# Kernel optimization log

Hardware: AMD Instinct MI355X
Metric: run time of the kernel (lower is better)

The kernel has to match this reference:

```python
import jax, jax.numpy as jnp
import numpy as np

SCALE_POS = 2.0
SCALE_NEG = 40.0
THRESH_POS = 0.5
THRESH_NEG = 0.5
MARGIN = 0.1
EPS = 1e-5


def setup_inputs() -> dict:
    key = jax.random.key(0)
    kf, kl = jax.random.split(key)
    B, D, NUM_CLASSES = 4096, 1024, 64
    feats = jax.random.normal(kf, (B, D), dtype=jnp.float32)
    feats = feats / jnp.linalg.norm(feats, axis=1, keepdims=True)  # L2-normalized embeddings
    labels = jax.random.randint(kl, (B,), 0, NUM_CLASSES, dtype=jnp.int64)
    return {"feats": feats, "labels": labels}


def reference(feats, labels):
    B = feats.shape[0]
    sim = jnp.matmul(feats, feats.T)  # [B, B]
    same = labels[:, None] == labels[None, :]
    pos_mask = same & (sim < 1.0 - EPS)  # drop self / near-duplicate pairs
    neg_mask = ~same

    # hard mining: keep negatives above min positive - margin, positives below max negative + margin
    min_pos = jnp.min(jnp.where(pos_mask, sim, jnp.inf), axis=1)   # [B]
    max_neg = jnp.max(jnp.where(neg_mask, sim, -jnp.inf), axis=1)  # [B]
    neg_sel = neg_mask & (sim + MARGIN > min_pos[:, None])
    pos_sel = pos_mask & (sim - MARGIN < max_neg[:, None])

    pos_sum = jnp.sum(jnp.where(pos_sel, jnp.exp(-SCALE_POS * (sim - THRESH_POS)), 0.0), axis=1)
    neg_sum = jnp.sum(jnp.where(neg_sel, jnp.exp(SCALE_NEG * (sim - THRESH_NEG)), 0.0), axis=1)
    pos_loss = jnp.log1p(pos_sum) / SCALE_POS
    neg_loss = jnp.log1p(neg_sum) / SCALE_NEG

    valid = jnp.any(pos_sel, axis=1) & jnp.any(neg_sel, axis=1)  # rows skipped by original loop
    return jnp.sum(jnp.where(valid, pos_loss + neg_loss, 0.0)) / B
```

## Files before the change

### kernel.cpp

```cpp
#include <hip/hip_runtime.h>

typedef _Float16 half8 __attribute__((ext_vector_type(8)));
typedef float floatx4 __attribute__((ext_vector_type(4)));
typedef int intx4 __attribute__((ext_vector_type(4)));
typedef int intx8 __attribute__((ext_vector_type(8)));
typedef __attribute__((address_space(1))) const void gvoid;
typedef __attribute__((address_space(3))) void svoid;

#define SCALE_POS 2.0f
#define SCALE_NEG 40.0f
#define THRESH 0.5f
#define MARGIN 0.1f
#define EPSV 1e-5f

__global__ void k_init(const float* __restrict__ feats,
                       unsigned char* __restrict__ f8,
                       float* __restrict__ out,
                       int total4) {
    int i = blockIdx.x * blockDim.x + threadIdx.x;
    if (i < total4) {
        float4 v = ((const float4*)feats)[i];
        int w = 0;
        w = __builtin_amdgcn_cvt_pk_fp8_f32(v.x, v.y, w, false);
        w = __builtin_amdgcn_cvt_pk_fp8_f32(v.z, v.w, w, true);
        ((int*)f8)[i] = w;
    }
    if (i == 0) out[0] = 0.f;
}

__global__ void __launch_bounds__(256, 4)
k_gemm_h(const unsigned char* __restrict__ f8,
         const int* __restrict__ labels,
         float* __restrict__ pmin,
         float* __restrict__ pmax,
         _Float16* __restrict__ simh,
         int D, int nb) {
    __shared__ __align__(16) unsigned char As[128 * 128];
    __shared__ __align__(16) unsigned char Bs[128 * 128];
    __shared__ int labR[128], labC[128];

    const int bid0 = blockIdx.x;
    const int t = (bid0 & 7) * 66 + (bid0 >> 3);
    int rb = 0, rem = t;
    while (rem >= nb - rb) { rem -= nb - rb; ++rb; }
    const int cb = rb + rem;
    const int rowBase = rb * 128;
    const int colBase = cb * 128;

    const int tid = threadIdx.x;
    const int lane = tid & 63;
    const int wave = tid >> 6;
    const int wr = wave >> 1;
    const int wc = wave & 1;
    const int q = lane >> 4;
    const int cIn = lane & 15;

    if (tid < 128) labR[tid] = labels[rowBase + tid];
    else           labC[tid - 128] = labels[colBase + (tid - 128)];

    const int subrow = lane >> 3;
    const int swz = (lane & 7) ^ subrow;
    const unsigned char* gP[8];
    unsigned char* lP[8];
#pragma unroll
    for (int j = 0; j < 8; ++j) {
        const int c = wave * 8 + j;
        const int grow = (c < 16) ? (rowBase + c * 8 + subrow)
                                  : (colBase + (c - 16) * 8 + subrow);
        gP[j] = f8 + (size_t)grow * D + swz * 16;
        lP[j] = ((c < 16) ? (As + c * 1024) : (Bs + (c - 16) * 1024)) + lane * 16;
    }

    int aOff0[4], aOff1[4], bOff0[4], bOff1[4];
#pragma unroll
    for (int i = 0; i < 4; ++i) {
        const int rA = wr * 64 + i * 16 + cIn;
        aOff0[i] = rA * 128 + ((2 * q) ^ (rA & 7)) * 16;
        aOff1[i] = rA * 128 + ((2 * q + 1) ^ (rA & 7)) * 16;
        const int rB = wc * 64 + i * 16 + cIn;
        bOff0[i] = rB * 128 + ((2 * q) ^ (rB & 7)) * 16;
        bOff1[i] = rB * 128 + ((2 * q + 1) ^ (rB & 7)) * 16;
    }

    floatx4 acc[4][4] = {};

    const int KT = D >> 7;
    for (int kt = 0; kt < KT; ++kt) {
        const int kOff = kt * 128;
        __syncthreads();
#pragma unroll
        for (int j = 0; j < 8; ++j)
            __builtin_amdgcn_global_load_lds((gvoid*)(gP[j] + kOff), (svoid*)lP[j], 16, 0, 0);
        __syncthreads();

        intx8 a[4], b[4];
#pragma unroll
        for (int i = 0; i < 4; ++i) {
            intx4 lo = *(const intx4*)(As + aOff0[i]);
            intx4 hi = *(const intx4*)(As + aOff1[i]);
            a[i] = __builtin_shufflevector(lo, hi, 0, 1, 2, 3, 4, 5, 6, 7);
        }
#pragma unroll
        for (int i = 0; i < 4; ++i) {
            intx4 lo = *(const intx4*)(Bs + bOff0[i]);
            intx4 hi = *(const intx4*)(Bs + bOff1[i]);
            b[i] = __builtin_shufflevector(lo, hi, 0, 1, 2, 3, 4, 5, 6, 7);
        }
#pragma unroll
        for (int i = 0; i < 4; ++i)
#pragma unroll
            for (int j2 = 0; j2 < 4; ++j2)
                acc[i][j2] = __builtin_amdgcn_mfma_scale_f32_16x16x128_f8f6f4(
                    a[i], b[j2], acc[i][j2], 0, 0,
                    0, 0x7f7f7f7f,
                    0, 0x7f7f7f7f);
    }

    int rLabv[16];
#pragma unroll
    for (int mi = 0; mi < 4; ++mi)
#pragma unroll
        for (int rr = 0; rr < 4; ++rr)
            rLabv[mi * 4 + rr] = labR[wr * 64 + mi * 16 + q * 4 + rr];
    int cLabv[4];
#pragma unroll
    for (int ni = 0; ni < 4; ++ni)
        cLabv[ni] = labC[wc * 64 + ni * 16 + cIn];

    {
        half8* dst = (half8*)(simh + (size_t)(2 * t + wc) * 8192
                                   + (size_t)(wr * 64 + lane) * 64);
#pragma unroll
        for (int mi = 0; mi < 4; ++mi) {
            half8 h0, h1;
#pragma unroll
            for (int ni = 0; ni < 2; ++ni)
#pragma unroll
                for (int rr = 0; rr < 4; ++rr) {
                    h0[ni * 4 + rr] = (_Float16)acc[mi][ni][rr];
                    h1[ni * 4 + rr] = (_Float16)acc[mi][ni + 2][rr];
                }
            dst[mi * 2] = h0;
            dst[mi * 2 + 1] = h1;
        }
    }

    {
        const int slotR = 2 * cb + wc;
#pragma unroll
        for (int mi = 0; mi < 4; ++mi)
#pragma unroll
            for (int rr = 0; rr < 4; ++rr) {
                const int rLoc = wr * 64 + mi * 16 + q * 4 + rr;
                const int rLab = rLabv[mi * 4 + rr];
                float vmin = 1e30f, vmax = -1e30f;
#pragma unroll
                for (int ni = 0; ni < 4; ++ni) {
                    float s = acc[mi][ni][rr];
                    if (rLab == cLabv[ni]) {
                        if (s < 1.0f - EPSV) vmin = fminf(vmin, s);
                    } else {
                        vmax = fmaxf(vmax, s);
                    }
                }
#pragma unroll
                for (int off = 8; off; off >>= 1) {
                    vmin = fminf(vmin, __shfl_xor(vmin, off, 16));
                    vmax = fmaxf(vmax, __shfl_xor(vmax, off, 16));
                }
                if (cIn == 0) {
                    pmin[(size_t)(rowBase + rLoc) * 64 + slotR] = vmin;
                    pmax[(size_t)(rowBase + rLoc) * 64 + slotR] = vmax;
                }
            }
    }

    if (rb != cb) {
        const int slotC = 2 * rb + wr;
#pragma unroll
        for (int ni = 0; ni < 4; ++ni) {
            const int cLab = cLabv[ni];
            float vmin = 1e30f, vmax = -1e30f;
#pragma unroll
            for (int mi = 0; mi < 4; ++mi)
#pragma unroll
                for (int rr = 0; rr < 4; ++rr) {
                    float s = acc[mi][ni][rr];
                    if (rLabv[mi * 4 + rr] == cLab) {
                        if (s < 1.0f - EPSV) vmin = fminf(vmin, s);
                    } else {
                        vmax = fmaxf(vmax, s);
                    }
                }
            vmin = fminf(vmin, __shfl_xor(vmin, 16, 64));
            vmin = fminf(vmin, __shfl_xor(vmin, 32, 64));
            vmax = fmaxf(vmax, __shfl_xor(vmax, 16, 64));
            vmax = fmaxf(vmax, __shfl_xor(vmax, 32, 64));
            if (q == 0) {
                const int cLoc = wc * 64 + ni * 16 + cIn;
                pmin[(size_t)(colBase + cLoc) * 64 + slotC] = vmin;
                pmax[(size_t)(colBase + cLoc) * 64 + slotC] = vmax;
            }
        }
    }
}

__global__ void __launch_bounds__(256)
k_sum2f(const _Float16* __restrict__ simh,
        const int* __restrict__ labels,
        const float* __restrict__ pmin,
        const float* __restrict__ pmax,
        float* __restrict__ psP, float* __restrict__ psN,
        int nb, int B) {
    __shared__ int labR[128], labC[128];
    __shared__ float gNR[128], gPR[128], gNC[128], gPC[128];

    int t = blockIdx.x;
    int rb = 0, rem = t;
    while (rem >= nb - rb) { rem -= nb - rb; ++rb; }
    const int cb = rb + rem;
    const int rowBase = rb * 128;

    const int tid = threadIdx.x;
    const int sub = tid >> 7;
    const int stid = tid & 127;
    const int wave = stid >> 6;
    const int lane = tid & 63;
    const int q = lane >> 4;
    const int cIn = lane & 15;
    const int colBase = cb * 128 + sub * 64;

    {
        const int j = tid & 127;
        const int base = (tid < 128) ? (rowBase + j) : (cb * 128 + j);
        const floatx4* pm = (const floatx4*)(pmin + (size_t)base * 64);
        const floatx4* px = (const floatx4*)(pmax + (size_t)base * 64);
        float mn = 1e30f, mx = -1e30f;
#pragma unroll
        for (int k = 0; k < 16; ++k) {
            floatx4 a = pm[k];
            floatx4 b = px[k];
            mn = fminf(mn, fminf(fminf(a[0], a[1]), fminf(a[2], a[3])));
            mx = fmaxf(mx, fmaxf(fmaxf(b[0], b[1]), fmaxf(b[2], b[3])));
        }
        if (tid < 128) {
            labR[j] = labels[rowBase + j];
            gNR[j] = mn - MARGIN;
            gPR[j] = mx + MARGIN;
        } else {
            labC[j] = labels[cb * 128 + j];
            gNC[j] = mn - MARGIN;
            gPC[j] = mx + MARGIN;
        }
    }
    __syncthreads();

    int cLabv[4];
    float gNCv[4], gPCv[4];
#pragma unroll
    for (int ni = 0; ni < 4; ++ni) {
        const int j = sub * 64 + ni * 16 + cIn;
        cLabv[ni] = labC[j];
        gNCv[ni] = gNC[j];
        gPCv[ni] = gPC[j];
    }

    const half8* src = (const half8*)(simh + (size_t)(2 * t + sub) * 8192 + (size_t)stid * 64);
    half8 hv[8];
#pragma unroll
    for (int v = 0; v < 8; ++v) hv[v] = src[v];

    float cps[4] = {}, cns[4] = {};
    const bool offd = (rb != cb);

    const int slotR = 2 * cb + sub;

#pragma unroll
    for (int mi = 0; mi < 4; ++mi)
#pragma unroll
        for (int rr = 0; rr < 4; ++rr) {
            const int rLoc = wave * 64 + mi * 16 + q * 4 + rr;
            const int rLab = labR[rLoc];
            const float gn = gNR[rLoc];
            const float gp = gPR[rLoc];
            float rp = 0.f, rn = 0.f;
#pragma unroll
            for (int ni = 0; ni < 4; ++ni) {
                const int idx = mi * 16 + ni * 4 + rr;
                const float s = (float)hv[idx >> 3][idx & 7];
                if (rLab == cLabv[ni]) {
                    if (s < 1.0f - EPSV) {
                        float ev = __expf(-SCALE_POS * (s - THRESH));
                        if (s < gp) rp += ev;
                        if (offd && s < gPCv[ni]) cps[ni] += ev;
                    }
                } else {
                    float ev = __expf(SCALE_NEG * (s - THRESH));
                    if (s > gn) rn += ev;
                    if (offd && s > gNCv[ni]) cns[ni] += ev;
                }
            }
#pragma unroll
            for (int off = 8; off; off >>= 1) {
                rp += __shfl_xor(rp, off, 16);
                rn += __shfl_xor(rn, off, 16);
            }
            if (cIn == 0) {
                psP[(size_t)(rowBase + rLoc) * 64 + slotR] = rp;
                psN[(size_t)(rowBase + rLoc) * 64 + slotR] = rn;
            }
        }
    if (offd) {
        const int slotC = 2 * rb + wave;
#pragma unroll
        for (int ni = 0; ni < 4; ++ni) {
            cps[ni] += __shfl_xor(cps[ni], 16, 64);
            cps[ni] += __shfl_xor(cps[ni], 32, 64);
            cns[ni] += __shfl_xor(cns[ni], 16, 64);
            cns[ni] += __shfl_xor(cns[ni], 32, 64);
            if (q == 0) {
                const int cLoc = ni * 16 + cIn;
                psP[(size_t)(colBase + cLoc) * 64 + slotC] = cps[ni];
                psN[(size_t)(colBase + cLoc) * 64 + slotC] = cns[ni];
            }
        }
    }
}

__global__ void __launch_bounds__(256)
k_final(const float* __restrict__ psP, const float* __restrict__ psN,
        float* __restrict__ out, int B) {
    __shared__ float red[4];
    const int r = blockIdx.x * 256 + threadIdx.x;
    const floatx4* pp = (const floatx4*)(psP + (size_t)r * 64);
    const floatx4* pn = (const floatx4*)(psN + (size_t)r * 64);
    float P = 0.f, N = 0.f;
#pragma unroll
    for (int k = 0; k < 16; ++k) {
        floatx4 a = pp[k];
        P += (a[0] + a[1]) + (a[2] + a[3]);
        floatx4 b = pn[k];
        N += (b[0] + b[1]) + (b[2] + b[3]);
    }
    float a = (P > 0.f && N > 0.f)
                  ? log1pf(P) * (1.0f / SCALE_POS) + log1pf(N) * (1.0f / SCALE_NEG)
                  : 0.f;
#pragma unroll
    for (int off = 32; off; off >>= 1) a += __shfl_down(a, off, 64);
    const int tid = threadIdx.x;
    if ((tid & 63) == 0) red[tid >> 6] = a;
    __syncthreads();
    if (tid == 0)
        atomicAdd(out, (red[0] + red[1] + red[2] + red[3]) / (float)B);
}

extern "C" void kernel_launch(void* const* d_in, const int* in_sizes, int n_in,
                              void* d_out, int out_size, void* d_ws, size_t ws_size,
                              hipStream_t stream) {
    const float* feats = (const float*)d_in[0];
    const int* labels = (const int*)d_in[1];
    const int B = in_sizes[1];
    const int D = in_sizes[0] / B;
    const int nb = B / 128;
    const int NT = nb * (nb + 1) / 2;
    const int total4 = B * D / 4;

    char* ws = (char*)d_ws;
    unsigned char* f8 = (unsigned char*)ws;
    size_t off = (size_t)B * D;
    float* pmin = (float*)(ws + off); off += (size_t)64 * B * 4;
    float* pmax = (float*)(ws + off); off += (size_t)64 * B * 4;
    float* psP  = (float*)(ws + off); off += (size_t)64 * B * 4;
    float* psN  = (float*)(ws + off); off += (size_t)64 * B * 4;
    _Float16* simh = (_Float16*)(ws + ((off + 255) & ~(size_t)255));
    float* outp = (float*)d_out;

    k_init<<<(total4 + 255) / 256, 256, 0, stream>>>(feats, f8, outp, total4);

    k_gemm_h<<<NT, 256, 0, stream>>>(f8, labels, pmin, pmax, simh, D, nb);

    k_sum2f<<<NT, 256, 0, stream>>>(simh, labels, pmin, pmax, psP, psN, nb, B);

    k_final<<<B / 256, 256, 0, stream>>>(psP, psN, outp, B);
}
```

Baseline: 136.3 us.

## Recompute FP8 similarity GEMM in second pass instead of storing fp16 tiles

The first GEMM pass no longer writes the fp16 similarity matrix to global memory. A second kernel recomputes the same FP8 MFMA tile GEMM and applies the exp-sum mining directly on the accumulators. This trades roughly 32MB of fp16 write plus read traffic for a second K-loop of matrix math. The second pass also sums the fp32 accumulators instead of fp16-rounded values, so precision slightly improves.

```diff
diff --git a/kernel.cpp b/kernel.cpp
--- a/kernel.cpp
+++ b/kernel.cpp
@@ -1,6 +1,5 @@
 #include <hip/hip_runtime.h>
 
-typedef _Float16 half8 __attribute__((ext_vector_type(8)));
 typedef float floatx4 __attribute__((ext_vector_type(4)));
 typedef int intx4 __attribute__((ext_vector_type(4)));
 typedef int intx8 __attribute__((ext_vector_type(8)));
@@ -29,12 +28,11 @@
 }
 
 __global__ void __launch_bounds__(256, 4)
-k_gemm_h(const unsigned char* __restrict__ f8,
-         const int* __restrict__ labels,
-         float* __restrict__ pmin,
-         float* __restrict__ pmax,
-         _Float16* __restrict__ simh,
-         int D, int nb) {
+k_gemmA(const unsigned char* __restrict__ f8,
+        const int* __restrict__ labels,
+        float* __restrict__ pmin,
+        float* __restrict__ pmax,
+        int D, int nb) {
     __shared__ __align__(16) unsigned char As[128 * 128];
     __shared__ __align__(16) unsigned char Bs[128 * 128];
     __shared__ int labR[128], labC[128];
@@ -112,8 +110,7 @@
             for (int j2 = 0; j2 < 4; ++j2)
                 acc[i][j2] = __builtin_amdgcn_mfma_scale_f32_16x16x128_f8f6f4(
                     a[i], b[j2], acc[i][j2], 0, 0,
-                    0, 0x7f7f7f7f,
-                    0, 0x7f7f7f7f);
+                    0, 0x7f7f7f7f, 0, 0x7f7f7f7f);
     }
 
     int rLabv[16];
@@ -126,24 +123,6 @@
 #pragma unroll
     for (int ni = 0; ni < 4; ++ni)
         cLabv[ni] = labC[wc * 64 + ni * 16 + cIn];
-
-    {
-        half8* dst = (half8*)(simh + (size_t)(2 * t + wc) * 8192
-                                   + (size_t)(wr * 64 + lane) * 64);
-#pragma unroll
-        for (int mi = 0; mi < 4; ++mi) {
-            half8 h0, h1;
-#pragma unroll
-            for (int ni = 0; ni < 2; ++ni)
-#pragma unroll
-                for (int rr = 0; rr < 4; ++rr) {
-                    h0[ni * 4 + rr] = (_Float16)acc[mi][ni][rr];
-                    h1[ni * 4 + rr] = (_Float16)acc[mi][ni + 2][rr];
-                }
-            dst[mi * 2] = h0;
-            dst[mi * 2 + 1] = h1;
-        }
-    }
 
     {
         const int slotR = 2 * cb + wc;
@@ -205,34 +184,38 @@
     }
 }
 
-__global__ void __launch_bounds__(256)
-k_sum2f(const _Float16* __restrict__ simh,
+__global__ void __launch_bounds__(256, 4)
+k_gemmB(const unsigned char* __restrict__ f8,
         const int* __restrict__ labels,
         const float* __restrict__ pmin,
         const float* __restrict__ pmax,
-        float* __restrict__ psP, float* __restrict__ psN,
-        int nb, int B) {
+        float* __restrict__ psP,
+        float* __restrict__ psN,
+        int D, int nb) {
+    __shared__ __align__(16) unsigned char As[128 * 128];
+    __shared__ __align__(16) unsigned char Bs[128 * 128];
     __shared__ int labR[128], labC[128];
     __shared__ float gNR[128], gPR[128], gNC[128], gPC[128];
 
-    int t = blockIdx.x;
+    const int bid0 = blockIdx.x;
+    const int t = (bid0 & 7) * 66 + (bid0 >> 3);
     int rb = 0, rem = t;
     while (rem >= nb - rb) { rem -= nb - rb; ++rb; }
     const int cb = rb + rem;
     const int rowBase = rb * 128;
+    const int colBase = cb * 128;
 
     const int tid = threadIdx.x;
-    const int sub = tid >> 7;
-    const int stid = tid & 127;
-    const int wave = stid >> 6;
     const int lane = tid & 63;
+    const int wave = tid >> 6;
+    const int wr = wave >> 1;
+    const int wc = wave & 1;
     const int q = lane >> 4;
     const int cIn = lane & 15;
-    const int colBase = cb * 128 + sub * 64;
 
     {
         const int j = tid & 127;
-        const int base = (tid < 128) ? (rowBase + j) : (cb * 128 + j);
+        const int base = (tid < 128) ? (rowBase + j) : (colBase + j);
         const floatx4* pm = (const floatx4*)(pmin + (size_t)base * 64);
         const floatx4* px = (const floatx4*)(pmax + (size_t)base * 64);
         float mn = 1e30f, mx = -1e30f;
@@ -248,46 +231,101 @@
             gNR[j] = mn - MARGIN;
             gPR[j] = mx + MARGIN;
         } else {
-            labC[j] = labels[cb * 128 + j];
+            labC[j] = labels[colBase + j];
             gNC[j] = mn - MARGIN;
             gPC[j] = mx + MARGIN;
         }
     }
-    __syncthreads();
-
+
+    const int subrow = lane >> 3;
+    const int swz = (lane & 7) ^ subrow;
+    const unsigned char* gP[8];
+    unsigned char* lP[8];
+#pragma unroll
+    for (int j = 0; j < 8; ++j) {
+        const int c = wave * 8 + j;
+        const int grow = (c < 16) ? (rowBase + c * 8 + subrow)
+                                  : (colBase + (c - 16) * 8 + subrow);
+        gP[j] = f8 + (size_t)grow * D + swz * 16;
+        lP[j] = ((c < 16) ? (As + c * 1024) : (Bs + (c - 16) * 1024)) + lane * 16;
+    }
+
+    int aOff0[4], aOff1[4], bOff0[4], bOff1[4];
+#pragma unroll
+    for (int i = 0; i < 4; ++i) {
+        const int rA = wr * 64 + i * 16 + cIn;
+        aOff0[i] = rA * 128 + ((2 * q) ^ (rA & 7)) * 16;
+        aOff1[i] = rA * 128 + ((2 * q + 1) ^ (rA & 7)) * 16;
+        const int rB = wc * 64 + i * 16 + cIn;
+        bOff0[i] = rB * 128 + ((2 * q) ^ (rB & 7)) * 16;
+        bOff1[i] = rB * 128 + ((2 * q + 1) ^ (rB & 7)) * 16;
+    }
+
+    floatx4 acc[4][4] = {};
+
+    const int KT = D >> 7;
+    for (int kt = 0; kt < KT; ++kt) {
+        const int kOff = kt * 128;
+        __syncthreads();
+#pragma unroll
+        for (int j = 0; j < 8; ++j)
+            __builtin_amdgcn_global_load_lds((gvoid*)(gP[j] + kOff), (svoid*)lP[j], 16, 0, 0);
+        __syncthreads();
+
+        intx8 a[4], b[4];
+#pragma unroll
+        for (int i = 0; i < 4; ++i) {
+            intx4 lo = *(const intx4*)(As + aOff0[i]);
+            intx4 hi = *(const intx4*)(As + aOff1[i]);
+            a[i] = __builtin_shufflevector(lo, hi, 0, 1, 2, 3, 4, 5, 6, 7);
+        }
+#pragma unroll
+        for (int i = 0; i < 4; ++i) {
+            intx4 lo = *(const intx4*)(Bs + bOff0[i]);
+            intx4 hi = *(const intx4*)(Bs + bOff1[i]);
+            b[i] = __builtin_shufflevector(lo, hi, 0, 1, 2, 3, 4, 5, 6, 7);
+        }
+#pragma unroll
+        for (int i = 0; i < 4; ++i)
+#pragma unroll
+            for (int j2 = 0; j2 < 4; ++j2)
+                acc[i][j2] = __builtin_amdgcn_mfma_scale_f32_16x16x128_f8f6f4(
+                    a[i], b[j2], acc[i][j2], 0, 0,
+                    0, 0x7f7f7f7f, 0, 0x7f7f7f7f);
+    }
+
+    int rLabv[16];
+#pragma unroll
+    for (int mi = 0; mi < 4; ++mi)
+#pragma unroll
+        for (int rr = 0; rr < 4; ++rr)
+            rLabv[mi * 4 + rr] = labR[wr * 64 + mi * 16 + q * 4 + rr];
     int cLabv[4];
     float gNCv[4], gPCv[4];
 #pragma unroll
     for (int ni = 0; ni < 4; ++ni) {
-        const int j = sub * 64 + ni * 16 + cIn;
+        const int j = wc * 64 + ni * 16 + cIn;
         cLabv[ni] = labC[j];
         gNCv[ni] = gNC[j];
         gPCv[ni] = gPC[j];
     }
 
-    const half8* src = (const half8*)(simh + (size_t)(2 * t + sub) * 8192 + (size_t)stid * 64);
-    half8 hv[8];
-#pragma unroll
-    for (int v = 0; v < 8; ++v) hv[v] = src[v];
-
+    const bool offd = (rb != cb);
     float cps[4] = {}, cns[4] = {};
-    const bool offd = (rb != cb);
-
-    const int slotR = 2 * cb + sub;
+    const int slotR = 2 * cb + wc;
 
 #pragma unroll
     for (int mi = 0; mi < 4; ++mi)
 #pragma unroll
         for (int rr = 0; rr < 4; ++rr) {
-            const int rLoc = wave * 64 + mi * 16 + q * 4 + rr;
-            const int rLab = labR[rLoc];
+            const int rLoc = wr * 64 + mi * 16 + q * 4 + rr;
+            const int rLab = rLabv[mi * 4 + rr];
             const float gn = gNR[rLoc];
             const float gp = gPR[rLoc];
             float rp = 0.f, rn = 0.f;
 #pragma unroll
             for (int ni = 0; ni < 4; ++ni) {
-                const int idx = mi * 16 + ni * 4 + rr;
-                const float s = (float)hv[idx >> 3][idx & 7];
+                const float s = acc[mi][ni][rr];
                 if (rLab == cLabv[ni]) {
                     if (s < 1.0f - EPSV) {
                         float ev = __expf(-SCALE_POS * (s - THRESH));
@@ -311,7 +349,7 @@
             }
         }
     if (offd) {
-        const int slotC = 2 * rb + wave;
+        const int slotC = 2 * rb + wr;
 #pragma unroll
         for (int ni = 0; ni < 4; ++ni) {
             cps[ni] += __shfl_xor(cps[ni], 16, 64);
@@ -319,7 +357,7 @@
             cns[ni] += __shfl_xor(cns[ni], 16, 64);
             cns[ni] += __shfl_xor(cns[ni], 32, 64);
             if (q == 0) {
-                const int cLoc = ni * 16 + cIn;
+                const int cLoc = wc * 64 + ni * 16 + cIn;
                 psP[(size_t)(colBase + cLoc) * 64 + slotC] = cps[ni];
                 psN[(size_t)(colBase + cLoc) * 64 + slotC] = cns[ni];
             }
@@ -372,14 +410,13 @@
     float* pmax = (float*)(ws + off); off += (size_t)64 * B * 4;
     float* psP  = (float*)(ws + off); off += (size_t)64 * B * 4;
     float* psN  = (float*)(ws + off); off += (size_t)64 * B * 4;
-    _Float16* simh = (_Float16*)(ws + ((off + 255) & ~(size_t)255));
     float* outp = (float*)d_out;
 
     k_init<<<(total4 + 255) / 256, 256, 0, stream>>>(feats, f8, outp, total4);
 
-    k_gemm_h<<<NT, 256, 0, stream>>>(f8, labels, pmin, pmax, simh, D, nb);
-
-    k_sum2f<<<NT, 256, 0, stream>>>(simh, labels, pmin, pmax, psP, psN, nb, B);
+    k_gemmA<<<NT, 256, 0, stream>>>(f8, labels, pmin, pmax, D, nb);
+
+    k_gemmB<<<NT, 256, 0, stream>>>(f8, labels, pmin, pmax, psP, psN, D, nb);
 
     k_final<<<B / 256, 256, 0, stream>>>(psP, psN, outp, B);
 }
```

Result: slower. 151.4 us (+11.1%).
